# Kernel optimization log

Measured on AMD Instinct MI355X. Metric: run time of the kernel, lower is better.

Reference implementation:

```python
import jax, jax.numpy as jnp
import numpy as np

HID = 512  # in_proj output width


def _segment_sizes(seq_len):
    # mirrors torch: periods = 1/rfftfreq(seq_len)[1:]; (periods+1e-5).int().unique()[::-1]
    freqs = np.fft.rfftfreq(seq_len)[1:]
    periods = 1.0 / freqs
    return np.unique((periods + 1e-5).astype(np.int32))[::-1]


def setup_inputs() -> dict:
    key = jax.random.key(0)
    ks = jax.random.split(key, 6)
    B, T, C, H, W, D = 16, 96, 3, 16, 16, 64
    NF = T // 2                      # num_freqs = 48
    S = len(_segment_sizes(T))       # 17 segment sizes
    x = jax.random.normal(ks[0], (B, T, C, H, W, D), jnp.float32)
    in_w = jax.random.normal(ks[1], (HID, C * D), jnp.float32) * 0.05
    in_b = jax.random.normal(ks[2], (HID,), jnp.float32) * 0.05
    w_gate = jax.random.normal(ks[3], (NF, S), jnp.float32) * 0.05
    w_noise = jax.random.normal(ks[4], (NF, S), jnp.float32) * 0.05
    noise = jax.random.normal(ks[5], (B, HID, S), jnp.float32)  # stands in for randn_like(clean_logits)
    return {"x": x, "in_w": in_w, "in_b": in_b, "w_gate": w_gate,
            "w_noise": w_noise, "noise": noise, "training": 1, "top_k": 3}


def reference(x, in_w, in_b, w_gate, w_noise, noise, training, top_k):
    B, T, C, H, W, D = x.shape
    noise_epsilon = 0.01
    # rearrange b t c h w d -> b t (h w) (c d); mean over (h w)
    xm = x.mean(axis=(3, 4)).reshape(B, T, C * D)          # [B,T,C*D]
    h = xm @ in_w.T + in_b                                  # [B,T,512]
    h = jnp.swapaxes(h, 1, 2)                               # [B,512,T]
    xf = jnp.fft.rfft(h, axis=-1, norm="ortho")[:, :, 1:]  # drop DC -> [B,512,T//2]
    amp = jnp.abs(xf)
    clean_logits = jnp.einsum("bdf,fs->bds", amp, w_gate)   # [B,512,S]
    if training:
        noise_stddev = jax.nn.softplus(jnp.einsum("bdf,fs->bds", amp, w_noise)) + noise_epsilon
        logits = clean_logits + noise * noise_stddev
    else:
        logits = clean_logits
    weights = logits.mean(axis=1)                           # [B,S]
    top_w, top_i = jax.lax.top_k(weights, top_k)            # [B,k]
    top_w = jax.nn.softmax(top_w, axis=-1)
    gates = jnp.zeros_like(weights).at[jnp.arange(B)[:, None], top_i].set(top_w)
    return gates
```

## Files before the change

### kernel.cpp

```cpp
#include <hip/hip_runtime.h>
#include <hip/hip_bf16.h>
#include <math.h>

#define NB 16
#define NT 96
#define NC 3
#define ND 64
#define NJ 192
#define NHID 512
#define NF 48
#define NS 17

__global__ __launch_bounds__(256) void k_mean(const float* __restrict__ x,
                                              float* __restrict__ xm) {
    const int blk = blockIdx.x;
    const int tid = threadIdx.x;
    const float4* xin = reinterpret_cast<const float4*>(x) + (size_t)blk * 4096;
    float4 acc = make_float4(0.f, 0.f, 0.f, 0.f);
#pragma unroll
    for (int k = 0; k < 16; ++k) {
        float4 v = xin[k * 256 + tid];
        acc.x += v.x; acc.y += v.y; acc.z += v.z; acc.w += v.w;
    }
    __shared__ float4 sums[256];
    sums[tid] = acc;
    __syncthreads();
    if (tid < 16) {
        float4 tot = make_float4(0.f, 0.f, 0.f, 0.f);
#pragma unroll
        for (int g = 0; g < 16; ++g) {
            float4 v = sums[g * 16 + tid];
            tot.x += v.x; tot.y += v.y; tot.z += v.z; tot.w += v.w;
        }
        const float s = 1.0f / 256.0f;
        tot.x *= s; tot.y *= s; tot.z *= s; tot.w *= s;
        const int c  = blk % NC;
        const int bt = blk / NC;
        float4* out = reinterpret_cast<float4*>(xm + (size_t)bt * NJ + c * ND);
        out[tid] = tot;
    }
}

__global__ __launch_bounds__(192) void k_dft(const float* __restrict__ xm,
                                             float2* __restrict__ PT) {
    const int b  = blockIdx.x / NF;
    const int jc = blockIdx.x % NF;
    const int tid = threadIdx.x;
    const int f  = tid % 48;
    const int jj = tid / 48;
    __shared__ float xs[NT][4];
    for (int i = tid; i < NT * 4; i += 192) {
        const int t = i >> 2, j4 = i & 3;
        xs[t][j4] = xm[((size_t)b * NT + t) * NJ + jc * 4 + j4];
    }
    __syncthreads();
    const float th = (2.0f * 3.14159265358979323846f / 96.0f) * (float)(f + 1);
    float s0, c0;
    sincosf(th, &s0, &c0);
    float c = 1.f, s = 0.f;
    float re = 0.f, im = 0.f;
    for (int t = 0; t < NT; ++t) {
        const float xv = xs[t][jj];
        re = fmaf(xv, c, re);
        im = fmaf(xv, s, im);
        const float cn = c * c0 - s * s0;
        s = s * c0 + c * s0;
        c = cn;
    }
    const float inv = 0.1020620726159657f;
    const int j = jc * 4 + jj;
    PT[((size_t)b * NJ + j) * NF + f] = make_float2(re * inv, -im * inv);
}

__global__ __launch_bounds__(192) void k_amp(const float* __restrict__ in_w,
                                             const float2* __restrict__ PT,
                                             float* __restrict__ amp) {
    const int b  = blockIdx.x >> 4;
    const int ot = blockIdx.x & 15;
    const int tid = threadIdx.x;
    const int og = tid & 7;
    const int fg = tid >> 3;
    __shared__ float wcT[NJ][36];
    for (int k = 0; k < 32; ++k) {
        wcT[tid][k] = in_w[(size_t)(ot * 32 + k) * NJ + tid];
    }
    __syncthreads();
    const float2* ptb = PT + (size_t)b * NJ * NF;
    float re0[4] = {0.f,0.f,0.f,0.f}, im0[4] = {0.f,0.f,0.f,0.f};
    float re1[4] = {0.f,0.f,0.f,0.f}, im1[4] = {0.f,0.f,0.f,0.f};
#pragma unroll 4
    for (int j = 0; j < NJ; ++j) {
        const float4 p  = *reinterpret_cast<const float4*>(&ptb[(size_t)j * NF + fg * 2]);
        const float4 w4 = *reinterpret_cast<const float4*>(&wcT[j][og * 4]);
        const float wv[4] = {w4.x, w4.y, w4.z, w4.w};
#pragma unroll
        for (int r = 0; r < 4; ++r) {
            re0[r] = fmaf(wv[r], p.x, re0[r]);
            im0[r] = fmaf(wv[r], p.y, im0[r]);
            re1[r] = fmaf(wv[r], p.z, re1[r]);
            im1[r] = fmaf(wv[r], p.w, im1[r]);
        }
    }
#pragma unroll
    for (int r = 0; r < 4; ++r) {
        const int o = ot * 32 + og * 4 + r;
        float2 a;
        a.x = sqrtf(re0[r] * re0[r] + im0[r] * im0[r]);
        a.y = sqrtf(re1[r] * re1[r] + im1[r] * im1[r]);
        *reinterpret_cast<float2*>(&amp[((size_t)b * NHID + o) * NF + fg * 2]) = a;
    }
}

__global__ __launch_bounds__(512) void k_weights(const float* __restrict__ amp,
                                                 const float* __restrict__ w_gate,
                                                 const float* __restrict__ w_noise,
                                                 const float* __restrict__ noise,
                                                 const int* __restrict__ training,
                                                 const int* __restrict__ top_k,
                                                 float* __restrict__ out) {
    const int b = blockIdx.x;
    const int tid = threadIdx.x;
    __shared__ float wg[NF * 20];
    __shared__ float wn[NF * 20];
    for (int i = tid; i < NF * 20; i += 512) {
        const int ff = i / 20, s = i % 20;
        wg[i] = (s < NS) ? w_gate[ff * NS + s] : 0.f;
        wn[i] = (s < NS) ? w_noise[ff * NS + s] : 0.f;
    }
    __syncthreads();

    const float4* a4 = reinterpret_cast<const float4*>(amp + ((size_t)b * NHID + tid) * NF);
    float aC[NS], aN[NS];
#pragma unroll
    for (int s = 0; s < NS; ++s) { aC[s] = 0.f; aN[s] = 0.f; }
    for (int q = 0; q < NF / 4; ++q) {
        float4 av = a4[q];
        float a[4] = {av.x, av.y, av.z, av.w};
#pragma unroll
        for (int u = 0; u < 4; ++u) {
            const int ff = q * 4 + u;
#pragma unroll
            for (int s = 0; s < NS; ++s) {
                aC[s] = fmaf(a[u], wg[ff * 20 + s], aC[s]);
                aN[s] = fmaf(a[u], wn[ff * 20 + s], aN[s]);
            }
        }
    }
    const int tr = training[0];
    const float* nrow = noise + ((size_t)b * NHID + tid) * NS;
#pragma unroll
    for (int s = 0; s < NS; ++s) {
        if (tr) {
            float xx = aN[s];
            float sp = fmaxf(xx, 0.f) + log1pf(expf(-fabsf(xx)));
            aC[s] += nrow[s] * (sp + 0.01f);
        }
    }
#pragma unroll
    for (int s = 0; s < NS; ++s) {
#pragma unroll
        for (int off = 1; off <= 32; off <<= 1)
            aC[s] += __shfl_xor(aC[s], off);
    }
    __shared__ float red[8][NS];
    __shared__ float wfin[NS];
    const int wave = tid >> 6;
    const int lane = tid & 63;
    if (lane == 0) {
#pragma unroll
        for (int s = 0; s < NS; ++s) red[wave][s] = aC[s];
    }
    __syncthreads();
    if (tid < NS) {
        float sum = 0.f;
#pragma unroll
        for (int w = 0; w < 8; ++w) sum += red[w][tid];
        wfin[tid] = sum * (1.0f / 512.0f);
    }
    __syncthreads();
    if (tid == 0) {
        int k = top_k[0];
        if (k < 1) k = 1;
        if (k > NS) k = NS;
        float w[NS];
#pragma unroll
        for (int s = 0; s < NS; ++s) w[s] = wfin[s];
        float tv[NS];
        int   ti[NS];
        int used = 0;
        for (int kk = 0; kk < k; ++kk) {
            float best = -INFINITY;
            int bi = 0;
#pragma unroll
            for (int s = 0; s < NS; ++s) {
                if (!((used >> s) & 1) && w[s] > best) { best = w[s]; bi = s; }
            }
            tv[kk] = best; ti[kk] = bi; used |= (1 << bi);
        }
        const float m = tv[0];
        float sum = 0.f;
        for (int kk = 0; kk < k; ++kk) { tv[kk] = expf(tv[kk] - m); sum += tv[kk]; }
        float outv[NS];
#pragma unroll
        for (int s = 0; s < NS; ++s) outv[s] = 0.f;
        for (int kk = 0; kk < k; ++kk) outv[ti[kk]] = tv[kk] / sum;
#pragma unroll
        for (int s = 0; s < NS; ++s) out[b * NS + s] = outv[s];
    }
}

extern "C" void kernel_launch(void* const* d_in, const int* in_sizes, int n_in,
                              void* d_out, int out_size, void* d_ws, size_t ws_size,
                              hipStream_t stream) {
    const float* x        = (const float*)d_in[0];
    const float* in_w     = (const float*)d_in[1];
    const float* w_gate   = (const float*)d_in[3];
    const float* w_noise  = (const float*)d_in[4];
    const float* noise    = (const float*)d_in[5];
    const int*   training = (const int*)d_in[6];
    const int*   top_k    = (const int*)d_in[7];
    float* out = (float*)d_out;

    float* ws  = (float*)d_ws;
    float*  xm = ws;
    float2* PT = (float2*)(xm + (size_t)NB * NT * NJ);
    float* amp = (float*)(PT + (size_t)NB * NJ * NF);

    k_mean   <<<NB * NT * NC, 256, 0, stream>>>(x, xm);
    k_dft    <<<NB * NF,      192, 0, stream>>>(xm, PT);
    k_amp    <<<NB * 16,      192, 0, stream>>>(in_w, PT, amp);
    k_weights<<<NB,           512, 0, stream>>>(amp, w_gate, w_noise, noise, training, top_k, out);
}
```

Baseline: 95.81 us.

## Fuse gate/noise projection into amplitude kernel and add tiny final top-k kernel

The amplitude kernel now keeps its 32x48 amplitude tile in shared memory and immediately applies the gate and noise projections, softplus and noise term. It writes per-block partial sums of the logits over its 32 hidden channels instead of the full amplitude tensor. A single-block final kernel sums the 16 partials per batch and does top-k and softmax. This removes the amplitude round trip through global memory and the 16-block weights kernel, which had low parallelism. In exchange, each amp block does more work and uses more shared memory.

Result: faster. 84.27 us (-12.0%).

```diff
diff --git a/kernel.cpp b/kernel.cpp
--- a/kernel.cpp
+++ b/kernel.cpp
@@ -72,119 +72,129 @@
     PT[((size_t)b * NJ + j) * NF + f] = make_float2(re * inv, -im * inv);
 }
 
-__global__ __launch_bounds__(192) void k_amp(const float* __restrict__ in_w,
-                                             const float2* __restrict__ PT,
-                                             float* __restrict__ amp) {
+__global__ __launch_bounds__(192) void k_ampw(const float* __restrict__ in_w,
+                                              const float2* __restrict__ PT,
+                                              const float* __restrict__ w_gate,
+                                              const float* __restrict__ w_noise,
+                                              const float* __restrict__ noise,
+                                              const int* __restrict__ training,
+                                              float* __restrict__ wpart) {
     const int b  = blockIdx.x >> 4;
     const int ot = blockIdx.x & 15;
     const int tid = threadIdx.x;
-    const int og = tid & 7;
-    const int fg = tid >> 3;
     __shared__ float wcT[NJ][36];
-    for (int k = 0; k < 32; ++k) {
-        wcT[tid][k] = in_w[(size_t)(ot * 32 + k) * NJ + tid];
-    }
-    __syncthreads();
-    const float2* ptb = PT + (size_t)b * NJ * NF;
-    float re0[4] = {0.f,0.f,0.f,0.f}, im0[4] = {0.f,0.f,0.f,0.f};
-    float re1[4] = {0.f,0.f,0.f,0.f}, im1[4] = {0.f,0.f,0.f,0.f};
-#pragma unroll 4
-    for (int j = 0; j < NJ; ++j) {
-        const float4 p  = *reinterpret_cast<const float4*>(&ptb[(size_t)j * NF + fg * 2]);
-        const float4 w4 = *reinterpret_cast<const float4*>(&wcT[j][og * 4]);
-        const float wv[4] = {w4.x, w4.y, w4.z, w4.w};
-#pragma unroll
-        for (int r = 0; r < 4; ++r) {
-            re0[r] = fmaf(wv[r], p.x, re0[r]);
-            im0[r] = fmaf(wv[r], p.y, im0[r]);
-            re1[r] = fmaf(wv[r], p.z, re1[r]);
-            im1[r] = fmaf(wv[r], p.w, im1[r]);
-        }
-    }
-#pragma unroll
-    for (int r = 0; r < 4; ++r) {
-        const int o = ot * 32 + og * 4 + r;
-        float2 a;
-        a.x = sqrtf(re0[r] * re0[r] + im0[r] * im0[r]);
-        a.y = sqrtf(re1[r] * re1[r] + im1[r] * im1[r]);
-        *reinterpret_cast<float2*>(&amp[((size_t)b * NHID + o) * NF + fg * 2]) = a;
-    }
-}
-
-__global__ __launch_bounds__(512) void k_weights(const float* __restrict__ amp,
-                                                 const float* __restrict__ w_gate,
-                                                 const float* __restrict__ w_noise,
-                                                 const float* __restrict__ noise,
-                                                 const int* __restrict__ training,
-                                                 const int* __restrict__ top_k,
-                                                 float* __restrict__ out) {
-    const int b = blockIdx.x;
-    const int tid = threadIdx.x;
+    __shared__ float ampL[32][50];
     __shared__ float wg[NF * 20];
     __shared__ float wn[NF * 20];
-    for (int i = tid; i < NF * 20; i += 512) {
+    for (int k = 0; k < 32; ++k)
+        wcT[tid][k] = in_w[(size_t)(ot * 32 + k) * NJ + tid];
+    for (int i = tid; i < NF * 20; i += 192) {
         const int ff = i / 20, s = i % 20;
         wg[i] = (s < NS) ? w_gate[ff * NS + s] : 0.f;
         wn[i] = (s < NS) ? w_noise[ff * NS + s] : 0.f;
     }
     __syncthreads();
 
-    const float4* a4 = reinterpret_cast<const float4*>(amp + ((size_t)b * NHID + tid) * NF);
-    float aC[NS], aN[NS];
-#pragma unroll
-    for (int s = 0; s < NS; ++s) { aC[s] = 0.f; aN[s] = 0.f; }
-    for (int q = 0; q < NF / 4; ++q) {
-        float4 av = a4[q];
-        float a[4] = {av.x, av.y, av.z, av.w};
-#pragma unroll
-        for (int u = 0; u < 4; ++u) {
-            const int ff = q * 4 + u;
-#pragma unroll
-            for (int s = 0; s < NS; ++s) {
-                aC[s] = fmaf(a[u], wg[ff * 20 + s], aC[s]);
-                aN[s] = fmaf(a[u], wn[ff * 20 + s], aN[s]);
+    {
+        const int og = tid & 7;
+        const int fg = tid >> 3;
+        const float2* ptb = PT + (size_t)b * NJ * NF;
+        float re0[4] = {0.f,0.f,0.f,0.f}, im0[4] = {0.f,0.f,0.f,0.f};
+        float re1[4] = {0.f,0.f,0.f,0.f}, im1[4] = {0.f,0.f,0.f,0.f};
+#pragma unroll 4
+        for (int j = 0; j < NJ; ++j) {
+            const float4 p  = *reinterpret_cast<const float4*>(&ptb[(size_t)j * NF + fg * 2]);
+            const float4 w4 = *reinterpret_cast<const float4*>(&wcT[j][og * 4]);
+            const float wv[4] = {w4.x, w4.y, w4.z, w4.w};
+#pragma unroll
+            for (int r = 0; r < 4; ++r) {
+                re0[r] = fmaf(wv[r], p.x, re0[r]);
+                im0[r] = fmaf(wv[r], p.y, im0[r]);
+                re1[r] = fmaf(wv[r], p.z, re1[r]);
+                im1[r] = fmaf(wv[r], p.w, im1[r]);
             }
         }
+#pragma unroll
+        for (int r = 0; r < 4; ++r) {
+            float2 a;
+            a.x = sqrtf(re0[r] * re0[r] + im0[r] * im0[r]);
+            a.y = sqrtf(re1[r] * re1[r] + im1[r] * im1[r]);
+            *reinterpret_cast<float2*>(&ampL[og * 4 + r][fg * 2]) = a;
+        }
+    }
+    __syncthreads();
+
+    const int ol = tid & 31;
+    const int sg = tid >> 5;
+    float aC[3] = {0.f, 0.f, 0.f};
+    float aN[3] = {0.f, 0.f, 0.f};
+    for (int f = 0; f < NF; ++f) {
+        const float a = ampL[ol][f];
+#pragma unroll
+        for (int k = 0; k < 3; ++k) {
+            aC[k] = fmaf(a, wg[f * 20 + sg * 3 + k], aC[k]);
+            aN[k] = fmaf(a, wn[f * 20 + sg * 3 + k], aN[k]);
+        }
     }
     const int tr = training[0];
-    const float* nrow = noise + ((size_t)b * NHID + tid) * NS;
+    const int o = ot * 32 + ol;
+    float v[3];
+#pragma unroll
+    for (int k = 0; k < 3; ++k) {
+        const int s = sg * 3 + k;
+        float val = aC[k];
+        if (tr && s < NS) {
+            const float xx = aN[k];
+            const float sp = fmaxf(xx, 0.f) + log1pf(expf(-fabsf(xx)));
+            val += noise[((size_t)b * NHID + o) * NS + s] * (sp + 0.01f);
+        }
+        v[k] = val;
+    }
+#pragma unroll
+    for (int k = 0; k < 3; ++k) {
+#pragma unroll
+        for (int off = 1; off <= 16; off <<= 1)
+            v[k] += __shfl_xor(v[k], off);
+    }
+    if (ol == 0) {
+        float* wp = wpart + ((size_t)(b * 16 + ot)) * 18;
+#pragma unroll
+        for (int k = 0; k < 3; ++k) {
+            const int s = sg * 3 + k;
+            if (s < NS) wp[s] = v[k];
+        }
+    }
+}
+
+__global__ __launch_bounds__(256) void k_final(const float* __restrict__ wpart,
+                                               const int* __restrict__ top_k,
+                                               float* __restrict__ out) {
+    const int tid = threadIdx.x;
+    const int b  = tid >> 4;
+    const int ot = tid & 15;
+    float acc[NS];
+    const float* wp = wpart + ((size_t)(b * 16 + ot)) * 18;
+#pragma unroll
+    for (int s = 0; s < NS; ++s) acc[s] = wp[s];
 #pragma unroll
     for (int s = 0; s < NS; ++s) {
-        if (tr) {
-            float xx = aN[s];
-            float sp = fmaxf(xx, 0.f) + log1pf(expf(-fabsf(xx)));
-            aC[s] += nrow[s] * (sp + 0.01f);
-        }
-    }
-#pragma unroll
-    for (int s = 0; s < NS; ++s) {
-#pragma unroll
-        for (int off = 1; off <= 32; off <<= 1)
-            aC[s] += __shfl_xor(aC[s], off);
-    }
-    __shared__ float red[8][NS];
-    __shared__ float wfin[NS];
-    const int wave = tid >> 6;
-    const int lane = tid & 63;
-    if (lane == 0) {
-#pragma unroll
-        for (int s = 0; s < NS; ++s) red[wave][s] = aC[s];
-    }
-    __syncthreads();
-    if (tid < NS) {
-        float sum = 0.f;
-#pragma unroll
-        for (int w = 0; w < 8; ++w) sum += red[w][tid];
-        wfin[tid] = sum * (1.0f / 512.0f);
-    }
-    __syncthreads();
-    if (tid == 0) {
+#pragma unroll
+        for (int off = 1; off <= 8; off <<= 1)
+            acc[s] += __shfl_xor(acc[s], off);
+    }
+    __shared__ float wf[NB][NS];
+    if (ot == 0) {
+#pragma unroll
+        for (int s = 0; s < NS; ++s) wf[b][s] = acc[s] * (1.0f / 512.0f);
+    }
+    __syncthreads();
+    if (tid < NB) {
         int k = top_k[0];
         if (k < 1) k = 1;
         if (k > NS) k = NS;
         float w[NS];
 #pragma unroll
-        for (int s = 0; s < NS; ++s) w[s] = wfin[s];
+        for (int s = 0; s < NS; ++s) w[s] = wf[tid][s];
         float tv[NS];
         int   ti[NS];
         int used = 0;
@@ -205,7 +215,7 @@
         for (int s = 0; s < NS; ++s) outv[s] = 0.f;
         for (int kk = 0; kk < k; ++kk) outv[ti[kk]] = tv[kk] / sum;
 #pragma unroll
-        for (int s = 0; s < NS; ++s) out[b * NS + s] = outv[s];
+        for (int s = 0; s < NS; ++s) out[tid * NS + s] = outv[s];
     }
 }
 
@@ -221,13 +231,13 @@
     const int*   top_k    = (const int*)d_in[7];
     float* out = (float*)d_out;
 
-    float* ws  = (float*)d_ws;
-    float*  xm = ws;
-    float2* PT = (float2*)(xm + (size_t)NB * NT * NJ);
-    float* amp = (float*)(PT + (size_t)NB * NJ * NF);
-
-    k_mean   <<<NB * NT * NC, 256, 0, stream>>>(x, xm);
-    k_dft    <<<NB * NF,      192, 0, stream>>>(xm, PT);
-    k_amp    <<<NB * 16,      192, 0, stream>>>(in_w, PT, amp);
-    k_weights<<<NB,           512, 0, stream>>>(amp, w_gate, w_noise, noise, training, top_k, out);
-}
+    float* ws    = (float*)d_ws;
+    float*  xm   = ws;
+    float2* PT   = (float2*)(xm + (size_t)NB * NT * NJ);
+    float* wpart = (float*)(PT + (size_t)NB * NJ * NF);
+
+    k_mean <<<NB * NT * NC, 256, 0, stream>>>(x, xm);
+    k_dft  <<<NB * NF,      192, 0, stream>>>(xm, PT);
+    k_ampw <<<NB * 16,      192, 0, stream>>>(in_w, PT, w_gate, w_noise, noise, training, wpart);
+    k_final<<<1,            256, 0, stream>>>(wpart, top_k, out);
+}
```
